# Optimization experiments

Hardware: AMD Instinct MI355X
Metric: run time of the kernel (lower is better)

The kernel has to match this reference:

```python
import jax, jax.numpy as jnp
import numpy as np

LN_EPS = 1e-5

def setup_inputs() -> dict:
    key = jax.random.key(0)
    k1, k2, k3 = jax.random.split(key, 3)
    L, B, D = 2048, 8, 1024
    x = jax.random.normal(k1, (L, B, D), dtype=jnp.float32)
    c = jnp.zeros((B, D), dtype=jnp.float32)
    W = jax.random.normal(k2, (D, 3 * D), dtype=jnp.float32) * 0.02
    # bias init from _init_bias: u-bias 0, f-bias 0.5, r-bias 0
    b = jnp.concatenate([jnp.zeros(D), jnp.full((D,), 0.5), jnp.zeros(D)]).astype(jnp.float32)
    gamma = jnp.ones((D,), dtype=jnp.float32)
    beta = jnp.zeros((D,), dtype=jnp.float32)
    return {"x": x, "c": c, "W": W, "b": b, "gamma": gamma, "beta": beta}

def reference(x, c, W, b, gamma, beta):
    # LayerNorm over last dim
    mu = jnp.mean(x, axis=-1, keepdims=True)
    var = jnp.mean(jnp.square(x - mu), axis=-1, keepdims=True)
    x_norm = (x - mu) * jax.lax.rsqrt(var + LN_EPS) * gamma + beta
    # Fused u/f/r projection: [L,B,3D]
    ufr = jnp.einsum('lbd,de->lbe', x_norm, W) + b
    u, f, r = jnp.split(ufr, 3, axis=-1)
    f_gate = jax.nn.sigmoid(f)
    r_gate = jax.nn.sigmoid(r)
    # Linear recurrence c_t = f_t * c_{t-1} + (1-f_t) * u_t via scan over time
    def step(c_prev, fu):
        f_t, u_t = fu
        c_t = f_t * c_prev + (1.0 - f_t) * u_t
        return c_t, c_t
    last_c, c_stack = jax.lax.scan(step, c, (f_gate, u))
    hs = r_gate * jnp.tanh(c_stack) + (1.0 - r_gate) * x_norm
    return x + hs, last_c
```

## Files before the change

kernel.cpp:

```cpp
#include <hip/hip_runtime.h>
#include <hip/hip_bf16.h>


typedef unsigned short u16;
typedef __bf16 bf16x8 __attribute__((ext_vector_type(8)));
typedef float f32x4 __attribute__((ext_vector_type(4)));

#define L_DIM 2048
#define B_DIM 8
#define D_DIM 1024
#define M_DIM (L_DIM * B_DIM)
#define K_DIM D_DIM
#define N_DIM (3 * D_DIM)
#define NCH 32
#define CLEN (L_DIM / NCH)
#define NT (K_DIM / 64)

#define LDS_B 65536
#define LDS_DUMMY 131072
#define LDS_TOTAL 147456

__device__ __forceinline__ float bf2f(u16 h) {
    unsigned int u = ((unsigned int)h) << 16;
    float f;
    __builtin_memcpy(&f, &u, 4);
    return f;
}

__device__ __forceinline__ u16 f2bf(float f) {
    unsigned int u;
    __builtin_memcpy(&u, &f, 4);
    u = u + 0x7fff + ((u >> 16) & 1);
    return (u16)(u >> 16);
}

__device__ __forceinline__ void async16(void* lds, const void* g) {
    __builtin_amdgcn_global_load_lds(
        (const __attribute__((address_space(1))) void*)g,
        (__attribute__((address_space(3))) void*)lds, 16, 0, 0);
}

__global__ __launch_bounds__(256) void ln_kernel(const float* __restrict__ x,
                                                 const float* __restrict__ gamma,
                                                 const float* __restrict__ beta,
                                                 u16* __restrict__ xn,
                                                 float2* __restrict__ mrs) {
    int row = blockIdx.x;
    int tid = threadIdx.x;
    const float4* xr = (const float4*)(x + (size_t)row * D_DIM);
    float4 v = xr[tid];
    float s = v.x + v.y + v.z + v.w;
    float q = v.x * v.x + v.y * v.y + v.z * v.z + v.w * v.w;
    #pragma unroll
    for (int off = 32; off; off >>= 1) {
        s += __shfl_down(s, off);
        q += __shfl_down(q, off);
    }
    __shared__ float ss[4], qq[4];
    int lane = tid & 63, wv = tid >> 6;
    if (lane == 0) { ss[wv] = s; qq[wv] = q; }
    __syncthreads();
    s = ss[0] + ss[1] + ss[2] + ss[3];
    q = qq[0] + qq[1] + qq[2] + qq[3];
    float mu = s * (1.0f / D_DIM);
    float var = q * (1.0f / D_DIM) - mu * mu;
    float rs = rsqrtf(var + 1e-5f);
    if (tid == 0) mrs[row] = make_float2(mu, rs);
    float4 g = ((const float4*)gamma)[tid];
    float4 bt = ((const float4*)beta)[tid];
    ushort4 o;
    o.x = f2bf((v.x - mu) * rs * g.x + bt.x);
    o.y = f2bf((v.y - mu) * rs * g.y + bt.y);
    o.z = f2bf((v.z - mu) * rs * g.z + bt.z);
    o.w = f2bf((v.w - mu) * rs * g.w + bt.w);
    ((ushort4*)(xn + (size_t)row * D_DIM))[tid] = o;
}

__global__ __launch_bounds__(256) void wt_kernel(const float* __restrict__ W,
                                                 u16* __restrict__ Wt) {
    __shared__ float t[64][65];
    int k0 = blockIdx.x * 64;
    int n0 = blockIdx.y * 64;
    int col = threadIdx.x & 63;
    int rg4 = threadIdx.x >> 6;
    #pragma unroll
    for (int j = 0; j < 16; ++j) {
        int r = rg4 * 16 + j;
        t[r][col] = W[(size_t)(k0 + r) * N_DIM + n0 + col];
    }
    __syncthreads();
    #pragma unroll
    for (int j = 0; j < 16; ++j) {
        int nr = rg4 * 16 + j;
        Wt[(size_t)(n0 + nr) * K_DIM + k0 + col] = f2bf(t[col][nr]);
    }
}

__global__ __launch_bounds__(512, 2) void gemm_kernel(const u16* __restrict__ A,
                                                      const u16* __restrict__ Bt,
                                                      const float* __restrict__ bias,
                                                      u16* __restrict__ uo,
                                                      u16* __restrict__ fo,
                                                      u16* __restrict__ ro) {
    extern __shared__ char lds[];
    const int tid = threadIdx.x;
    const int wave = tid >> 6, lane = tid & 63;
    const int lm = lane & 15, lg = lane >> 4;
    const int wm = wave >> 2, wn = wave & 3;
    const int m0 = blockIdx.x * 256;
    const int n0 = blockIdx.y * 256;

    const int xk0 = ((0 | lg) ^ (lm & 7)) << 4;
    const int xk1 = ((4 | lg) ^ (lm & 7)) << 4;
    const char* pA0 = lds + (wm * 128 + lm) * 128 + xk0;
    const char* pA1 = lds + (wm * 128 + lm) * 128 + xk1;
    const char* pB0 = lds + LDS_B + (wn * 64 + lm) * 128 + xk0;
    const char* pB1 = lds + LDS_B + (wn * 64 + lm) * 128 + xk1;

    const int c1 = 512 + tid;
    const int r0 = tid >> 3, cc0 = (tid & 7) ^ (r0 & 7);
    const int r1 = c1 >> 3, cc1 = (c1 & 7) ^ (r1 & 7);
    const char* gA0 = (const char*)A + ((size_t)(m0 + r0) * K_DIM + cc0 * 8) * 2;
    const char* gA1 = (const char*)A + ((size_t)(m0 + r1) * K_DIM + cc1 * 8) * 2;
    const char* gB0 = (const char*)Bt + ((size_t)(n0 + r0) * K_DIM + cc0 * 8) * 2;
    const char* gB1 = (const char*)Bt + ((size_t)(n0 + r1) * K_DIM + cc1 * 8) * 2;
    char* dstW = lds + wave * 1024;

    f32x4 acc[8][4] = {};
    bf16x8 av[4], aw[4], bv0[4], bv1[4];

    auto stageA = [&](int t1, int h) {
        char* dst = (t1 < NT) ? (dstW + ((t1 & 1) << 15) + (h << 14))
                              : (lds + LDS_DUMMY + wave * 1024);
        int ko = ((t1 & 15) << 7) + (h << 18);
        async16(dst,        gA0 + ko);
        async16(dst + 8192, gA1 + ko);
    };
    auto stageB = [&](int t2, int h) {
        char* dst = (t2 < NT) ? (dstW + LDS_B + ((t2 & 1) << 15) + (h << 14))
                              : (lds + LDS_DUMMY + wave * 1024);
        int ko = ((t2 & 15) << 7) + (h << 18);
        async16(dst,        gB0 + ko);
        async16(dst + 8192, gB1 + ko);
    };

#define LDA(dst, pbase, bb, mf0)                                                \
    do { _Pragma("unroll")                                                      \
        for (int q = 0; q < 4; ++q)                                             \
            dst[q] = *(const bf16x8*)(pbase + (bb) * 32768 + ((mf0) + q) * 2048); \
    } while (0)

#define LDB(dst, pbase, bb)                                                     \
    do { _Pragma("unroll")                                                      \
        for (int nf = 0; nf < 4; ++nf)                                          \
            dst[nf] = *(const bf16x8*)(pbase + (bb) * 32768 + nf * 2048);       \
    } while (0)

#define MFMA16(r0q, afr, bfr)                                                   \
    do { _Pragma("unroll")                                                      \
        for (int q = 0; q < 4; ++q)                                             \
            _Pragma("unroll")                                                   \
            for (int nf = 0; nf < 4; ++nf)                                      \
                acc[(r0q) + q][nf] = __builtin_amdgcn_mfma_f32_16x16x32_bf16(   \
                    afr[q], bfr[nf], acc[(r0q) + q][nf], 0, 0, 0);              \
    } while (0)

#define PH_SYNC()                                                               \
    do { __builtin_amdgcn_s_barrier();                                          \
         asm volatile("s_waitcnt lgkmcnt(0)");                                  \
         __builtin_amdgcn_sched_barrier(0); } while (0)

#define TILE_BODY(t, bb)                                                        \
    do {                                                                        \
                                                                   \
        LDA(av, pA0, bb, 0);                                                    \
        LDB(bv0, pB0, bb);                                                      \
        stageA((t) + 1, 0);                                                     \
        PH_SYNC();                                                              \
        __builtin_amdgcn_s_setprio(1);  MFMA16(0, av, bv0);                     \
        __builtin_amdgcn_s_setprio(0);  __builtin_amdgcn_s_barrier();           \
                                                                   \
        LDA(av, pA1, bb, 0);                                                    \
        LDB(bv1, pB1, bb);                                                      \
        stageA((t) + 1, 1);                                                     \
        PH_SYNC();                                                              \
        __builtin_amdgcn_s_setprio(1);  MFMA16(0, av, bv1);                     \
        __builtin_amdgcn_s_setprio(0);  __builtin_amdgcn_s_barrier();           \
                                                                   \
        LDA(aw, pA0, bb, 4);                                                    \
        stageB((t) + 2, 0);                                                     \
        PH_SYNC();                                                              \
        __builtin_amdgcn_s_setprio(1);  MFMA16(4, aw, bv0);                     \
        __builtin_amdgcn_s_setprio(0);  __builtin_amdgcn_s_barrier();           \
                                                                   \
        LDA(aw, pA1, bb, 4);                                                    \
        stageB((t) + 2, 1);                                                     \
        PH_SYNC();                                                              \
        __builtin_amdgcn_s_setprio(1);  MFMA16(4, aw, bv1);                     \
        __builtin_amdgcn_s_setprio(0);                                          \
        asm volatile("s_waitcnt vmcnt(4)" ::: "memory");                        \
        __builtin_amdgcn_s_barrier();                                           \
    } while (0)

    stageA(0, 0); stageA(0, 1);
    stageB(0, 0); stageB(0, 1);
    stageB(1, 0); stageB(1, 1);
    asm volatile("s_waitcnt vmcnt(4)" ::: "memory");
    __builtin_amdgcn_s_barrier();

    for (int t = 0; t < NT; t += 2) {
        TILE_BODY(t, 0);
        TILE_BODY(t + 1, 1);
    }

    int seg = n0 >> 10;
    u16* outp = (seg == 0) ? uo : ((seg == 1) ? fo : ro);
    float bb4[4];
    #pragma unroll
    for (int nf = 0; nf < 4; ++nf) bb4[nf] = bias[n0 + wn * 64 + nf * 16 + lm];
    const int cmb = (n0 + wn * 64 + lm) & 1023;
    #pragma unroll
    for (int mf = 0; mf < 8; ++mf) {
        #pragma unroll
        for (int j = 0; j < 4; ++j) {
            int row = m0 + wm * 128 + mf * 16 + lg * 4 + j;
            u16* rp = outp + (size_t)row * D_DIM + cmb;
            #pragma unroll
            for (int nf = 0; nf < 4; ++nf) {
                float val = acc[mf][nf][j] + bb4[nf];
                if (seg != 0) val = 1.0f / (1.0f + __expf(-val));
                rp[nf * 16] = f2bf(val);
            }
        }
    }
#undef LDA
#undef LDB
#undef MFMA16
#undef PH_SYNC
#undef TILE_BODY
}

__global__ __launch_bounds__(256) void scan1_kernel(const u16* __restrict__ fg,
                                                    const u16* __restrict__ u,
                                                    float* __restrict__ Aa,
                                                    float* __restrict__ Ss) {
    int ch = blockIdx.x;
    int bd = (blockIdx.y * 256 + threadIdx.x) * 2;
    int b = bd >> 10, d = bd & 1023;
    float a0 = 1.0f, a1 = 1.0f, s0 = 0.0f, s1 = 0.0f;
    for (int t = ch * CLEN; t < ch * CLEN + CLEN; ++t) {
        size_t idx = ((size_t)(t * B_DIM + b) << 10) + d;
        ushort2 f2 = *(const ushort2*)(fg + idx);
        ushort2 u2 = *(const ushort2*)(u + idx);
        float f0 = bf2f(f2.x), f1 = bf2f(f2.y);
        float v0 = bf2f(u2.x), v1 = bf2f(u2.y);
        s0 = f0 * s0 + (1.0f - f0) * v0;
        s1 = f1 * s1 + (1.0f - f1) * v1;
        a0 *= f0;
        a1 *= f1;
    }
    int o = ch * 8192 + bd;
    *(float2*)(Aa + o) = make_float2(a0, a1);
    *(float2*)(Ss + o) = make_float2(s0, s1);
}

__global__ __launch_bounds__(256) void scan2_kernel(const float* __restrict__ Aa,
                                                    const float* __restrict__ Ss,
                                                    const float* __restrict__ c0,
                                                    float* __restrict__ cs,
                                                    float* __restrict__ lastc) {
    int bd = blockIdx.x * 256 + threadIdx.x;
    float c = c0[bd];
    #pragma unroll 4
    for (int ch = 0; ch < NCH; ++ch) {
        cs[ch * 8192 + bd] = c;
        c = Aa[ch * 8192 + bd] * c + Ss[ch * 8192 + bd];
    }
    lastc[bd] = c;
}

__global__ __launch_bounds__(256) void scan3_kernel(const float* __restrict__ cs,
                                                    const u16* __restrict__ fg,
                                                    const u16* __restrict__ u,
                                                    const u16* __restrict__ rg,
                                                    const float2* __restrict__ mrs,
                                                    const float* __restrict__ gamma,
                                                    const float* __restrict__ beta,
                                                    const float* __restrict__ x,
                                                    float* __restrict__ out) {
    int ch = blockIdx.x;
    int bd = (blockIdx.y * 256 + threadIdx.x) * 2;
    int b = bd >> 10, d = bd & 1023;
    float2 gm = *(const float2*)(gamma + d);
    float2 bt = *(const float2*)(beta + d);
    float c0v = cs[ch * 8192 + bd];
    float c1v = cs[ch * 8192 + bd + 1];
    for (int t = ch * CLEN; t < ch * CLEN + CLEN; ++t) {
        size_t idx = ((size_t)(t * B_DIM + b) << 10) + d;
        ushort2 f2 = *(const ushort2*)(fg + idx);
        ushort2 u2 = *(const ushort2*)(u + idx);
        ushort2 r2 = *(const ushort2*)(rg + idx);
        float2 x2 = *(const float2*)(x + idx);
        float2 mr = mrs[t * B_DIM + b];
        float f0 = bf2f(f2.x), f1 = bf2f(f2.y);
        float v0 = bf2f(u2.x), v1 = bf2f(u2.y);
        float r0 = bf2f(r2.x), r1 = bf2f(r2.y);
        float n0 = (x2.x - mr.x) * mr.y * gm.x + bt.x;
        float n1 = (x2.y - mr.x) * mr.y * gm.y + bt.y;
        c0v = f0 * c0v + (1.0f - f0) * v0;
        c1v = f1 * c1v + (1.0f - f1) * v1;
        float h0 = r0 * tanhf(c0v) + (1.0f - r0) * n0;
        float h1 = r1 * tanhf(c1v) + (1.0f - r1) * n1;
        *(float2*)(out + idx) = make_float2(x2.x + h0, x2.y + h1);
    }
}

extern "C" void kernel_launch(void* const* d_in, const int* in_sizes, int n_in,
                              void* d_out, int out_size, void* d_ws, size_t ws_size,
                              hipStream_t stream) {
    const float* x     = (const float*)d_in[0];
    const float* c0    = (const float*)d_in[1];
    const float* W     = (const float*)d_in[2];
    const float* b     = (const float*)d_in[3];
    const float* gamma = (const float*)d_in[4];
    const float* beta  = (const float*)d_in[5];
    float* out = (float*)d_out;
    float* lastc = out + (size_t)M_DIM * D_DIM;

    char* w = (char*)d_ws;
    u16* xn = (u16*)w;  w += (size_t)M_DIM * D_DIM * 2;
    u16* Wt = (u16*)w;  w += (size_t)N_DIM * K_DIM * 2;
    u16* ug = (u16*)w;  w += (size_t)M_DIM * D_DIM * 2;
    u16* fg = (u16*)w;  w += (size_t)M_DIM * D_DIM * 2;
    u16* rg = (u16*)w;  w += (size_t)M_DIM * D_DIM * 2;
    float* Aa = (float*)w; w += (size_t)NCH * 8192 * 4;
    float* Ss = (float*)w; w += (size_t)NCH * 8192 * 4;
    float* cs = (float*)w; w += (size_t)NCH * 8192 * 4;
    float2* mrs = (float2*)w; w += (size_t)M_DIM * 8;

    hipFuncSetAttribute(reinterpret_cast<const void*>(gemm_kernel),
                        hipFuncAttributeMaxDynamicSharedMemorySize, LDS_TOTAL);

    ln_kernel<<<M_DIM, 256, 0, stream>>>(x, gamma, beta, xn, mrs);
    wt_kernel<<<dim3(K_DIM / 64, N_DIM / 64), 256, 0, stream>>>(W, Wt);
    gemm_kernel<<<dim3(M_DIM / 256, N_DIM / 256), 512, LDS_TOTAL, stream>>>(xn, Wt, b, ug, fg, rg);
    scan1_kernel<<<dim3(NCH, 16), 256, 0, stream>>>(fg, ug, Aa, Ss);
    scan2_kernel<<<32, 256, 0, stream>>>(Aa, Ss, c0, cs, lastc);
    scan3_kernel<<<dim3(NCH, 16), 256, 0, stream>>>(cs, fg, ug, rg, mrs, gamma, beta, x, out);
}
```

Baseline: 200.1 us.

## Halve GEMM N-tile and single-buffer B tile to raise occupancy

Halves the GEMM block's N-tile from 256 to 128 columns. The B operand becomes a single 16KB buffer, loaded one tile ahead instead of two, and the dummy LDS slot is dropped in favour of early returns. LDS per block falls from 144KB to 80KB and accumulator registers are halved, so more workgroups can be resident per CU; launch bounds now request 4. The cost is twice as many blocks re-reading A, a full vmcnt(0) wait at each tile end that exposes load latency, and a lower ratio of MFMA work to LDS traffic per wave.

```diff
diff --git a/kernel.cpp b/kernel.cpp
--- a/kernel.cpp
+++ b/kernel.cpp
@@ -16,9 +16,8 @@
 #define CLEN (L_DIM / NCH)
 #define NT (K_DIM / 64)
 
-#define LDS_B 65536
-#define LDS_DUMMY 131072
-#define LDS_TOTAL 147456
+#define LDS_B_OFF 65536
+#define LDS_TOTAL 81920
 
 __device__ __forceinline__ float bf2f(u16 h) {
     unsigned int u = ((unsigned int)h) << 16;
@@ -96,7 +95,7 @@
     }
 }
 
-__global__ __launch_bounds__(512, 2) void gemm_kernel(const u16* __restrict__ A,
+__global__ __launch_bounds__(512, 4) void gemm_kernel(const u16* __restrict__ A,
                                                       const u16* __restrict__ Bt,
                                                       const float* __restrict__ bias,
                                                       u16* __restrict__ uo,
@@ -108,14 +107,14 @@
     const int lm = lane & 15, lg = lane >> 4;
     const int wm = wave >> 2, wn = wave & 3;
     const int m0 = blockIdx.x * 256;
-    const int n0 = blockIdx.y * 256;
+    const int n0 = blockIdx.y * 128;
 
     const int xk0 = ((0 | lg) ^ (lm & 7)) << 4;
     const int xk1 = ((4 | lg) ^ (lm & 7)) << 4;
     const char* pA0 = lds + (wm * 128 + lm) * 128 + xk0;
     const char* pA1 = lds + (wm * 128 + lm) * 128 + xk1;
-    const char* pB0 = lds + LDS_B + (wn * 64 + lm) * 128 + xk0;
-    const char* pB1 = lds + LDS_B + (wn * 64 + lm) * 128 + xk1;
+    const char* pB0 = lds + LDS_B_OFF + (wn * 32 + lm) * 128 + xk0;
+    const char* pB1 = lds + LDS_B_OFF + (wn * 32 + lm) * 128 + xk1;
 
     const int c1 = 512 + tid;
     const int r0 = tid >> 3, cc0 = (tid & 7) ^ (r0 & 7);
@@ -126,20 +125,20 @@
     const char* gB1 = (const char*)Bt + ((size_t)(n0 + r1) * K_DIM + cc1 * 8) * 2;
     char* dstW = lds + wave * 1024;
 
-    f32x4 acc[8][4] = {};
-    bf16x8 av[4], aw[4], bv0[4], bv1[4];
+    f32x4 acc[8][2] = {};
+    bf16x8 av[4], aw[4], bv0[2], bv1[2];
 
     auto stageA = [&](int t1, int h) {
-        char* dst = (t1 < NT) ? (dstW + ((t1 & 1) << 15) + (h << 14))
-                              : (lds + LDS_DUMMY + wave * 1024);
+        if (t1 >= NT) return;
+        char* dst = dstW + ((t1 & 1) << 15) + (h << 14);
         int ko = ((t1 & 15) << 7) + (h << 18);
         async16(dst,        gA0 + ko);
         async16(dst + 8192, gA1 + ko);
     };
-    auto stageB = [&](int t2, int h) {
-        char* dst = (t2 < NT) ? (dstW + LDS_B + ((t2 & 1) << 15) + (h << 14))
-                              : (lds + LDS_DUMMY + wave * 1024);
-        int ko = ((t2 & 15) << 7) + (h << 18);
+    auto stageB = [&](int t1) {
+        if (t1 >= NT) return;
+        char* dst = dstW + LDS_B_OFF;
+        int ko = (t1 & 15) << 7;
         async16(dst,        gB0 + ko);
         async16(dst + 8192, gB1 + ko);
     };
@@ -150,17 +149,17 @@
             dst[q] = *(const bf16x8*)(pbase + (bb) * 32768 + ((mf0) + q) * 2048); \
     } while (0)
 
-#define LDB(dst, pbase, bb)                                                     \
+#define LDB(dst, pbase)                                                         \
     do { _Pragma("unroll")                                                      \
-        for (int nf = 0; nf < 4; ++nf)                                          \
-            dst[nf] = *(const bf16x8*)(pbase + (bb) * 32768 + nf * 2048);       \
+        for (int nf = 0; nf < 2; ++nf)                                          \
+            dst[nf] = *(const bf16x8*)(pbase + nf * 2048);                      \
     } while (0)
 
-#define MFMA16(r0q, afr, bfr)                                                   \
+#define MFMA8(r0q, afr, bfr)                                                    \
     do { _Pragma("unroll")                                                      \
         for (int q = 0; q < 4; ++q)                                             \
             _Pragma("unroll")                                                   \
-            for (int nf = 0; nf < 4; ++nf)                                      \
+            for (int nf = 0; nf < 2; ++nf)                                      \
                 acc[(r0q) + q][nf] = __builtin_amdgcn_mfma_f32_16x16x32_bf16(   \
                     afr[q], bfr[nf], acc[(r0q) + q][nf], 0, 0, 0);              \
     } while (0)
@@ -174,40 +173,38 @@
     do {                                                                        \
                                                                    \
         LDA(av, pA0, bb, 0);                                                    \
-        LDB(bv0, pB0, bb);                                                      \
+        LDB(bv0, pB0);                                                          \
         stageA((t) + 1, 0);                                                     \
         PH_SYNC();                                                              \
-        __builtin_amdgcn_s_setprio(1);  MFMA16(0, av, bv0);                     \
+        __builtin_amdgcn_s_setprio(1);  MFMA8(0, av, bv0);                      \
         __builtin_amdgcn_s_setprio(0);  __builtin_amdgcn_s_barrier();           \
                                                                    \
         LDA(av, pA1, bb, 0);                                                    \
-        LDB(bv1, pB1, bb);                                                      \
+        LDB(bv1, pB1);                                                          \
         stageA((t) + 1, 1);                                                     \
         PH_SYNC();                                                              \
-        __builtin_amdgcn_s_setprio(1);  MFMA16(0, av, bv1);                     \
+        __builtin_amdgcn_s_setprio(1);  MFMA8(0, av, bv1);                      \
         __builtin_amdgcn_s_setprio(0);  __builtin_amdgcn_s_barrier();           \
-                                                                   \
+                          \
         LDA(aw, pA0, bb, 4);                                                    \
-        stageB((t) + 2, 0);                                                     \
+        stageB((t) + 1);                                                        \
         PH_SYNC();                                                              \
-        __builtin_amdgcn_s_setprio(1);  MFMA16(4, aw, bv0);                     \
+        __builtin_amdgcn_s_setprio(1);  MFMA8(4, aw, bv0);                      \
         __builtin_amdgcn_s_setprio(0);  __builtin_amdgcn_s_barrier();           \
                                                                    \
         LDA(aw, pA1, bb, 4);                                                    \
-        stageB((t) + 2, 1);                                                     \
         PH_SYNC();                                                              \
-        __builtin_amdgcn_s_setprio(1);  MFMA16(4, aw, bv1);                     \
+        __builtin_amdgcn_s_setprio(1);  MFMA8(4, aw, bv1);                      \
         __builtin_amdgcn_s_setprio(0);                                          \
-        asm volatile("s_waitcnt vmcnt(4)" ::: "memory");                        \
+        asm volatile("s_waitcnt vmcnt(0)" ::: "memory");                        \
         __builtin_amdgcn_s_barrier();                                           \
     } while (0)
 
-    stageA(0, 0); stageA(0, 1);
-    stageB(0, 0); stageB(0, 1);
-    stageB(1, 0); stageB(1, 1);
-    asm volatile("s_waitcnt vmcnt(4)" ::: "memory");
+    stageA(0, 0); stageA(0, 1); stageB(0);
+    asm volatile("s_waitcnt vmcnt(0)" ::: "memory");
     __builtin_amdgcn_s_barrier();
 
+    #pragma unroll 1
     for (int t = 0; t < NT; t += 2) {
         TILE_BODY(t, 0);
         TILE_BODY(t + 1, 1);
@@ -215,10 +212,10 @@
 
     int seg = n0 >> 10;
     u16* outp = (seg == 0) ? uo : ((seg == 1) ? fo : ro);
-    float bb4[4];
-    #pragma unroll
-    for (int nf = 0; nf < 4; ++nf) bb4[nf] = bias[n0 + wn * 64 + nf * 16 + lm];
-    const int cmb = (n0 + wn * 64 + lm) & 1023;
+    float bb2[2];
+    #pragma unroll
+    for (int nf = 0; nf < 2; ++nf) bb2[nf] = bias[n0 + wn * 32 + nf * 16 + lm];
+    const int cmb = (n0 + wn * 32 + lm) & 1023;
     #pragma unroll
     for (int mf = 0; mf < 8; ++mf) {
         #pragma unroll
@@ -226,8 +223,8 @@
             int row = m0 + wm * 128 + mf * 16 + lg * 4 + j;
             u16* rp = outp + (size_t)row * D_DIM + cmb;
             #pragma unroll
-            for (int nf = 0; nf < 4; ++nf) {
-                float val = acc[mf][nf][j] + bb4[nf];
+            for (int nf = 0; nf < 2; ++nf) {
+                float val = acc[mf][nf][j] + bb2[nf];
                 if (seg != 0) val = 1.0f / (1.0f + __expf(-val));
                 rp[nf * 16] = f2bf(val);
             }
@@ -235,7 +232,7 @@
     }
 #undef LDA
 #undef LDB
-#undef MFMA16
+#undef MFMA8
 #undef PH_SYNC
 #undef TILE_BODY
 }
@@ -343,7 +340,7 @@
 
     ln_kernel<<<M_DIM, 256, 0, stream>>>(x, gamma, beta, xn, mrs);
     wt_kernel<<<dim3(K_DIM / 64, N_DIM / 64), 256, 0, stream>>>(W, Wt);
-    gemm_kernel<<<dim3(M_DIM / 256, N_DIM / 256), 512, LDS_TOTAL, stream>>>(xn, Wt, b, ug, fg, rg);
+    gemm_kernel<<<dim3(M_DIM / 256, N_DIM / 128), 512, LDS_TOTAL, stream>>>(xn, Wt, b, ug, fg, rg);
     scan1_kernel<<<dim3(NCH, 16), 256, 0, stream>>>(fg, ug, Aa, Ss);
     scan2_kernel<<<32, 256, 0, stream>>>(Aa, Ss, c0, cs, lastc);
     scan3_kernel<<<dim3(NCH, 16), 256, 0, stream>>>(cs, fg, ug, rg, mrs, gamma, beta, x, out);
```

Result: slower. 206.9 us (+3.4%).

## Compute f/r gate projections with FP8 MFMA GEMM, keep u in bf16

Applied to the files above, without the earlier changes.

Splits the fused projection GEMM in two. The u-projection stays on the bf16 MFMA path. The f and r gate projections now run through a new FP8 (e4m3) GEMM kernel that uses 16x16x32 fp8 MFMA, with W pre-scaled by 64 and the accumulator rescaled afterwards. The layernorm kernel also writes an FP8 copy of x_norm, staged temporarily in the output buffer. This halves operand bytes and uses the faster FP8 matrix rate for two thirds of the GEMM, at the cost of reduced gate precision and an extra kernel launch and quantized write.

```diff
diff --git a/kernel.cpp b/kernel.cpp
--- a/kernel.cpp
+++ b/kernel.cpp
@@ -1,8 +1,10 @@
 #include <hip/hip_runtime.h>
 #include <hip/hip_bf16.h>
+#include <hip/hip_fp8.h>
 
 
 typedef unsigned short u16;
+typedef unsigned char u8;
 typedef __bf16 bf16x8 __attribute__((ext_vector_type(8)));
 typedef float f32x4 __attribute__((ext_vector_type(4)));
 
@@ -19,6 +21,9 @@
 #define LDS_B 65536
 #define LDS_DUMMY 131072
 #define LDS_TOTAL 147456
+#define L8_B 32768
+#define L8_DUMMY 65536
+#define L8_TOTAL 73728
 
 __device__ __forceinline__ float bf2f(u16 h) {
     unsigned int u = ((unsigned int)h) << 16;
@@ -34,6 +39,11 @@
     return (u16)(u >> 16);
 }
 
+__device__ __forceinline__ u8 f2e4(float v) {
+    __hip_fp8_e4m3 t(v);
+    return (u8)t.__x;
+}
+
 __device__ __forceinline__ void async16(void* lds, const void* g) {
     __builtin_amdgcn_global_load_lds(
         (const __attribute__((address_space(1))) void*)g,
@@ -44,6 +54,7 @@
                                                  const float* __restrict__ gamma,
                                                  const float* __restrict__ beta,
                                                  u16* __restrict__ xn,
+                                                 u8* __restrict__ xq,
                                                  float2* __restrict__ mrs) {
     int row = blockIdx.x;
     int tid = threadIdx.x;
@@ -68,16 +79,21 @@
     if (tid == 0) mrs[row] = make_float2(mu, rs);
     float4 g = ((const float4*)gamma)[tid];
     float4 bt = ((const float4*)beta)[tid];
+    float n0 = (v.x - mu) * rs * g.x + bt.x;
+    float n1 = (v.y - mu) * rs * g.y + bt.y;
+    float n2 = (v.z - mu) * rs * g.z + bt.z;
+    float n3 = (v.w - mu) * rs * g.w + bt.w;
     ushort4 o;
-    o.x = f2bf((v.x - mu) * rs * g.x + bt.x);
-    o.y = f2bf((v.y - mu) * rs * g.y + bt.y);
-    o.z = f2bf((v.z - mu) * rs * g.z + bt.z);
-    o.w = f2bf((v.w - mu) * rs * g.w + bt.w);
+    o.x = f2bf(n0); o.y = f2bf(n1); o.z = f2bf(n2); o.w = f2bf(n3);
     ((ushort4*)(xn + (size_t)row * D_DIM))[tid] = o;
+    uchar4 o8;
+    o8.x = f2e4(n0); o8.y = f2e4(n1); o8.z = f2e4(n2); o8.w = f2e4(n3);
+    ((uchar4*)(xq + (size_t)row * D_DIM))[tid] = o8;
 }
 
 __global__ __launch_bounds__(256) void wt_kernel(const float* __restrict__ W,
-                                                 u16* __restrict__ Wt) {
+                                                 u16* __restrict__ Wt,
+                                                 u8* __restrict__ Wf8) {
     __shared__ float t[64][65];
     int k0 = blockIdx.x * 64;
     int n0 = blockIdx.y * 64;
@@ -89,19 +105,25 @@
         t[r][col] = W[(size_t)(k0 + r) * N_DIM + n0 + col];
     }
     __syncthreads();
-    #pragma unroll
-    for (int j = 0; j < 16; ++j) {
-        int nr = rg4 * 16 + j;
-        Wt[(size_t)(n0 + nr) * K_DIM + k0 + col] = f2bf(t[col][nr]);
+    if (n0 < 1024) {
+        #pragma unroll
+        for (int j = 0; j < 16; ++j) {
+            int nr = rg4 * 16 + j;
+            Wt[(size_t)(n0 + nr) * K_DIM + k0 + col] = f2bf(t[col][nr]);
+        }
+    } else {
+        #pragma unroll
+        for (int j = 0; j < 16; ++j) {
+            int nr = rg4 * 16 + j;
+            Wf8[(size_t)(n0 - 1024 + nr) * K_DIM + k0 + col] = f2e4(t[col][nr] * 64.0f);
+        }
     }
 }
 
 __global__ __launch_bounds__(512, 2) void gemm_kernel(const u16* __restrict__ A,
                                                       const u16* __restrict__ Bt,
                                                       const float* __restrict__ bias,
-                                                      u16* __restrict__ uo,
-                                                      u16* __restrict__ fo,
-                                                      u16* __restrict__ ro) {
+                                                      u16* __restrict__ uo) {
     extern __shared__ char lds[];
     const int tid = threadIdx.x;
     const int wave = tid >> 6, lane = tid & 63;
@@ -172,27 +194,23 @@
 
 #define TILE_BODY(t, bb)                                                        \
     do {                                                                        \
-                                                                   \
         LDA(av, pA0, bb, 0);                                                    \
         LDB(bv0, pB0, bb);                                                      \
         stageA((t) + 1, 0);                                                     \
         PH_SYNC();                                                              \
         __builtin_amdgcn_s_setprio(1);  MFMA16(0, av, bv0);                     \
         __builtin_amdgcn_s_setprio(0);  __builtin_amdgcn_s_barrier();           \
-                                                                   \
         LDA(av, pA1, bb, 0);                                                    \
         LDB(bv1, pB1, bb);                                                      \
         stageA((t) + 1, 1);                                                     \
         PH_SYNC();                                                              \
         __builtin_amdgcn_s_setprio(1);  MFMA16(0, av, bv1);                     \
         __builtin_amdgcn_s_setprio(0);  __builtin_amdgcn_s_barrier();           \
-                                                                   \
         LDA(aw, pA0, bb, 4);                                                    \
         stageB((t) + 2, 0);                                                     \
         PH_SYNC();                                                              \
         __builtin_amdgcn_s_setprio(1);  MFMA16(4, aw, bv0);                     \
         __builtin_amdgcn_s_setprio(0);  __builtin_amdgcn_s_barrier();           \
-                                                                   \
         LDA(aw, pA1, bb, 4);                                                    \
         stageB((t) + 2, 1);                                                     \
         PH_SYNC();                                                              \
@@ -213,11 +231,138 @@
         TILE_BODY(t + 1, 1);
     }
 
+    float bb4[4];
+    #pragma unroll
+    for (int nf = 0; nf < 4; ++nf) bb4[nf] = bias[n0 + wn * 64 + nf * 16 + lm];
+    const int cmb = n0 + wn * 64 + lm;
+    #pragma unroll
+    for (int mf = 0; mf < 8; ++mf) {
+        #pragma unroll
+        for (int j = 0; j < 4; ++j) {
+            int row = m0 + wm * 128 + mf * 16 + lg * 4 + j;
+            u16* rp = uo + (size_t)row * D_DIM + cmb;
+            #pragma unroll
+            for (int nf = 0; nf < 4; ++nf)
+                rp[nf * 16] = f2bf(acc[mf][nf][j] + bb4[nf]);
+        }
+    }
+#undef LDA
+#undef LDB
+#undef MFMA16
+#undef PH_SYNC
+#undef TILE_BODY
+}
+
+__global__ __launch_bounds__(512, 2) void gemm8_kernel(const u8* __restrict__ A8,
+                                                       const u8* __restrict__ B8,
+                                                       const float* __restrict__ bias,
+                                                       u16* __restrict__ fo,
+                                                       u16* __restrict__ ro) {
+    extern __shared__ char lds[];
+    const int tid = threadIdx.x;
+    const int wave = tid >> 6, lane = tid & 63;
+    const int lm = lane & 15, lg = lane >> 4;
+    const int wm = wave >> 2, wn = wave & 3;
+    const int m0 = blockIdx.x * 256;
+    const int n0 = blockIdx.y * 256;
+
+    const int sl = (lg & 1) * 8;
+    const int xq0 = (((0 + (lg >> 1)) ^ (lm & 3)) << 4) + sl;
+    const int xq1 = (((2 + (lg >> 1)) ^ (lm & 3)) << 4) + sl;
+    const char* pA0 = lds + (wm * 128 + lm) * 64 + xq0;
+    const char* pA1 = lds + (wm * 128 + lm) * 64 + xq1;
+    const char* pB0 = lds + L8_B + (wn * 64 + lm) * 64 + xq0;
+    const char* pB1 = lds + L8_B + (wn * 64 + lm) * 64 + xq1;
+
+    const int r0 = tid >> 2, cq0 = (tid & 3) ^ (r0 & 3);
+    const char* gA = (const char*)A8 + (size_t)(m0 + r0) * K_DIM + cq0 * 16;
+    const char* gB = (const char*)B8 + (size_t)(n0 + r0) * K_DIM + cq0 * 16;
+    char* dstW = lds + wave * 1024;
+
+    f32x4 acc[8][4] = {};
+    long av[4], aw[4], bv0[4], bv1[4];
+
+    auto stageA = [&](int t1, int h) {
+        char* dst = (t1 < NT) ? (dstW + ((t1 & 1) << 14) + (h << 13))
+                              : (lds + L8_DUMMY + wave * 1024);
+        async16(dst, gA + ((t1 & 15) << 6) + (h << 17));
+    };
+    auto stageB = [&](int t2, int h) {
+        char* dst = (t2 < NT) ? (dstW + L8_B + ((t2 & 1) << 14) + (h << 13))
+                              : (lds + L8_DUMMY + wave * 1024);
+        async16(dst, gB + ((t2 & 15) << 6) + (h << 17));
+    };
+
+#define LDA8(dst, pbase, bb, mf0)                                               \
+    do { _Pragma("unroll")                                                      \
+        for (int q = 0; q < 4; ++q)                                             \
+            dst[q] = *(const long*)(pbase + (bb) * 16384 + ((mf0) + q) * 1024); \
+    } while (0)
+
+#define LDB8(dst, pbase, bb)                                                    \
+    do { _Pragma("unroll")                                                      \
+        for (int nf = 0; nf < 4; ++nf)                                          \
+            dst[nf] = *(const long*)(pbase + (bb) * 16384 + nf * 1024);         \
+    } while (0)
+
+#define MFMA16F8(r0q, afr, bfr)                                                 \
+    do { _Pragma("unroll")                                                      \
+        for (int q = 0; q < 4; ++q)                                             \
+            _Pragma("unroll")                                                   \
+            for (int nf = 0; nf < 4; ++nf)                                      \
+                acc[(r0q) + q][nf] = __builtin_amdgcn_mfma_f32_16x16x32_fp8_fp8(\
+                    afr[q], bfr[nf], acc[(r0q) + q][nf], 0, 0, 0);              \
+    } while (0)
+
+#define PH_SYNC()                                                               \
+    do { __builtin_amdgcn_s_barrier();                                          \
+         asm volatile("s_waitcnt lgkmcnt(0)");                                  \
+         __builtin_amdgcn_sched_barrier(0); } while (0)
+
+#define TILE_BODY8(t, bb)                                                       \
+    do {                                                                        \
+        LDA8(av, pA0, bb, 0);                                                   \
+        LDB8(bv0, pB0, bb);                                                     \
+        stageA((t) + 1, 0);                                                     \
+        PH_SYNC();                                                              \
+        __builtin_amdgcn_s_setprio(1);  MFMA16F8(0, av, bv0);                   \
+        __builtin_amdgcn_s_setprio(0);  __builtin_amdgcn_s_barrier();           \
+        LDA8(av, pA1, bb, 0);                                                   \
+        LDB8(bv1, pB1, bb);                                                     \
+        stageA((t) + 1, 1);                                                     \
+        PH_SYNC();                                                              \
+        __builtin_amdgcn_s_setprio(1);  MFMA16F8(0, av, bv1);                   \
+        __builtin_amdgcn_s_setprio(0);  __builtin_amdgcn_s_barrier();           \
+        LDA8(aw, pA0, bb, 4);                                                   \
+        stageB((t) + 2, 0);                                                     \
+        PH_SYNC();                                                              \
+        __builtin_amdgcn_s_setprio(1);  MFMA16F8(4, aw, bv0);                   \
+        __builtin_amdgcn_s_setprio(0);  __builtin_amdgcn_s_barrier();           \
+        LDA8(aw, pA1, bb, 4);                                                   \
+        stageB((t) + 2, 1);                                                     \
+        PH_SYNC();                                                              \
+        __builtin_amdgcn_s_setprio(1);  MFMA16F8(4, aw, bv1);                   \
+        __builtin_amdgcn_s_setprio(0);                                          \
+        asm volatile("s_waitcnt vmcnt(2)" ::: "memory");                        \
+        __builtin_amdgcn_s_barrier();                                           \
+    } while (0)
+
+    stageA(0, 0); stageA(0, 1);
+    stageB(0, 0); stageB(0, 1);
+    stageB(1, 0); stageB(1, 1);
+    asm volatile("s_waitcnt vmcnt(2)" ::: "memory");
+    __builtin_amdgcn_s_barrier();
+
+    for (int t = 0; t < NT; t += 2) {
+        TILE_BODY8(t, 0);
+        TILE_BODY8(t + 1, 1);
+    }
+
     int seg = n0 >> 10;
-    u16* outp = (seg == 0) ? uo : ((seg == 1) ? fo : ro);
+    u16* outp = seg ? ro : fo;
     float bb4[4];
     #pragma unroll
-    for (int nf = 0; nf < 4; ++nf) bb4[nf] = bias[n0 + wn * 64 + nf * 16 + lm];
+    for (int nf = 0; nf < 4; ++nf) bb4[nf] = bias[1024 + n0 + wn * 64 + nf * 16 + lm];
     const int cmb = (n0 + wn * 64 + lm) & 1023;
     #pragma unroll
     for (int mf = 0; mf < 8; ++mf) {
@@ -227,17 +372,16 @@
             u16* rp = outp + (size_t)row * D_DIM + cmb;
             #pragma unroll
             for (int nf = 0; nf < 4; ++nf) {
-                float val = acc[mf][nf][j] + bb4[nf];
-                if (seg != 0) val = 1.0f / (1.0f + __expf(-val));
-                rp[nf * 16] = f2bf(val);
+                float val = acc[mf][nf][j] * 0.015625f + bb4[nf];
+                rp[nf * 16] = f2bf(1.0f / (1.0f + __expf(-val)));
             }
         }
     }
-#undef LDA
-#undef LDB
-#undef MFMA16
+#undef LDA8
+#undef LDB8
+#undef MFMA16F8
 #undef PH_SYNC
-#undef TILE_BODY
+#undef TILE_BODY8
 }
 
 __global__ __launch_bounds__(256) void scan1_kernel(const u16* __restrict__ fg,
@@ -326,6 +470,7 @@
     const float* beta  = (const float*)d_in[5];
     float* out = (float*)d_out;
     float* lastc = out + (size_t)M_DIM * D_DIM;
+    u8* xq = (u8*)d_out;
 
     char* w = (char*)d_ws;
     u16* xn = (u16*)w;  w += (size_t)M_DIM * D_DIM * 2;
@@ -337,13 +482,17 @@
     float* Ss = (float*)w; w += (size_t)NCH * 8192 * 4;
     float* cs = (float*)w; w += (size_t)NCH * 8192 * 4;
     float2* mrs = (float2*)w; w += (size_t)M_DIM * 8;
+    u8* Wf8 = (u8*)w; w += (size_t)2048 * K_DIM;
 
     hipFuncSetAttribute(reinterpret_cast<const void*>(gemm_kernel),
                         hipFuncAttributeMaxDynamicSharedMemorySize, LDS_TOTAL);
-
-    ln_kernel<<<M_DIM, 256, 0, stream>>>(x, gamma, beta, xn, mrs);
-    wt_kernel<<<dim3(K_DIM / 64, N_DIM / 64), 256, 0, stream>>>(W, Wt);
-    gemm_kernel<<<dim3(M_DIM / 256, N_DIM / 256), 512, LDS_TOTAL, stream>>>(xn, Wt, b, ug, fg, rg);
+    hipFuncSetAttribute(reinterpret_cast<const void*>(gemm8_kernel),
+                        hipFuncAttributeMaxDynamicSharedMemorySize, L8_TOTAL);
+
+    ln_kernel<<<M_DIM, 256, 0, stream>>>(x, gamma, beta, xn, xq, mrs);
+    wt_kernel<<<dim3(K_DIM / 64, N_DIM / 64), 256, 0, stream>>>(W, Wt, Wf8);
+    gemm_kernel<<<dim3(M_DIM / 256, 4), 512, LDS_TOTAL, stream>>>(xn, Wt, b, ug);
+    gemm8_kernel<<<dim3(M_DIM / 256, 8), 512, L8_TOTAL, stream>>>(xq, Wf8, b, fg, rg);
     scan1_kernel<<<dim3(NCH, 16), 256, 0, stream>>>(fg, ug, Aa, Ss);
     scan2_kernel<<<32, 256, 0, stream>>>(Aa, Ss, c0, cs, lastc);
     scan3_kernel<<<dim3(NCH, 16), 256, 0, stream>>>(cs, fg, ug, rg, mrs, gamma, beta, x, out);
```

Result: slower. 214.5 us (+7.2%).
